# Performance work log

Measured on AMD Instinct MI355X. Metric: run time of the kernel, lower is better.

The kernel has to match this reference:

```python
import jax, jax.numpy as jnp
import numpy as np

N = 8192      # nodes
E = 262144    # edges (avg degree 32)
NFEAT = 1024
NHID = 512
ZDIM = 32


def _uniform(key, shape, stdv):
    return jax.random.uniform(key, shape, jnp.float32, -stdv, stdv)


def setup_inputs() -> dict:
    key = jax.random.key(0)
    ks = jax.random.split(key, 10)
    x = jax.random.normal(ks[0], (N, NFEAT), jnp.float32)
    adj_rows = jnp.sort(jax.random.randint(ks[1], (E,), 0, N))
    adj_cols = jax.random.randint(ks[2], (E,), 0, N)
    # positive edge weights, roughly row-normalized (avg degree 32)
    adj_vals = jax.random.uniform(ks[3], (E,), jnp.float32) / 32.0
    s0 = 1.0 / np.sqrt(NHID).astype(np.float32)
    s1 = 1.0 / np.sqrt(ZDIM).astype(np.float32)
    W0 = _uniform(ks[4], (NFEAT, NHID), s0)
    b0 = _uniform(ks[5], (NHID,), s0)
    W1 = _uniform(ks[6], (NHID, ZDIM), s1)
    b1 = _uniform(ks[7], (ZDIM,), s1)
    W2 = _uniform(ks[8], (NHID, ZDIM), s1)
    b2 = _uniform(ks[9], (ZDIM,), s1)
    return dict(x=x, adj_vals=adj_vals, W0=W0, b0=b0, W1=W1, b1=b1,
                W2=W2, b2=b2, adj_rows=adj_rows, adj_cols=adj_cols)


def _spmm(rows, cols, vals, mat):
    # sparse [N,N] @ dense [N,D] via gather + segment_sum
    return jax.ops.segment_sum(vals[:, None] * mat[cols], rows, num_segments=N)


def reference(x, adj_vals, W0, b0, W1, b1, W2, b2, adj_rows, adj_cols):
    # GraphConvolution: spmm(adj, x @ W) + b  (eval mode: dropout is identity)
    h = jax.nn.relu(_spmm(adj_rows, adj_cols, adj_vals, x @ W0) + b0)
    mu = jax.nn.relu(_spmm(adj_rows, adj_cols, adj_vals, h @ W1) + b1)
    logvar = jax.nn.relu(_spmm(adj_rows, adj_cols, adj_vals, h @ W2) + b2)
    z = mu  # reparameterize in eval mode returns mu
    adj_recon = jax.nn.sigmoid(z @ z.T)  # [N, N] inner-product decoder
    return adj_recon, z, mu, logvar
```

## Files before the change

### kernel.cpp

```cpp
#include <hip/hip_runtime.h>
#include <hip/hip_bf16.h>

typedef __bf16 bf16_t;
typedef __bf16 bf16x8 __attribute__((ext_vector_type(8)));
typedef float f32x4 __attribute__((ext_vector_type(4)));

#define NN 8192
#define EE 262144
#define NF 1024
#define NH 512
#define ZD 32

__global__ __launch_bounds__(256) void k_cvt(const float* __restrict__ in,
                                             bf16_t* __restrict__ out, int n8) {
  int i = blockIdx.x * 256 + threadIdx.x;
  if (i >= n8) return;
  const float4 a = ((const float4*)in)[i * 2];
  const float4 b = ((const float4*)in)[i * 2 + 1];
  bf16x8 o;
  o[0] = (bf16_t)a.x; o[1] = (bf16_t)a.y; o[2] = (bf16_t)a.z; o[3] = (bf16_t)a.w;
  o[4] = (bf16_t)b.x; o[5] = (bf16_t)b.y; o[6] = (bf16_t)b.z; o[7] = (bf16_t)b.w;
  ((bf16x8*)out)[i] = o;
}

__global__ __launch_bounds__(256) void k_transpose_cvt(const float* __restrict__ in,
                                                       bf16_t* __restrict__ out,
                                                       int R, int C) {
  __shared__ float tile[32][33];
  const int c0 = blockIdx.x * 32, r0 = blockIdx.y * 32;
  const int tx = threadIdx.x & 31, ty = threadIdx.x >> 5;
  #pragma unroll
  for (int i = ty; i < 32; i += 8)
    tile[i][tx] = in[(size_t)(r0 + i) * C + (c0 + tx)];
  __syncthreads();
  #pragma unroll
  for (int i = ty; i < 32; i += 8)
    out[(size_t)(c0 + i) * R + (r0 + tx)] = (bf16_t)tile[tx][i];
}

__global__ void k_rowptr(const int* __restrict__ rows, int* __restrict__ rp,
                         int n, int e) {
  int r = blockIdx.x * 256 + threadIdx.x;
  if (r > n) return;
  if (r == n) { rp[n] = e; return; }
  int lo = 0, hi = e;
  while (lo < hi) { int mid = (lo + hi) >> 1; if (rows[mid] < r) lo = mid + 1; else hi = mid; }
  rp[r] = lo;
}

__global__ __launch_bounds__(256) void k_gemm_bt_128x128(
    const bf16_t* __restrict__ A, const bf16_t* __restrict__ Bt,
    float* __restrict__ C, int M, int N, int K) {
  __shared__ bf16_t As[128 * 32];
  __shared__ bf16_t Bs[128 * 32];
  const int tid = threadIdx.x;
  const int lane = tid & 63, wave = tid >> 6;
  const int wx = wave & 1, wy = wave >> 1;
  const int m0 = blockIdx.y * 128, n0 = blockIdx.x * 128;
  const int q = lane >> 4, ml = lane & 15;

  const int sr = tid >> 2, ss = tid & 3;
  const int sw_lo = sr * 32 + ((ss ^ (sr & 3)) * 8);
  const int sw_hi = sw_lo + 64 * 32;

  int a_off[4], b_off[4];
  #pragma unroll
  for (int i = 0; i < 4; ++i) {
    int m = wy * 64 + i * 16 + ml;
    a_off[i] = m * 32 + ((q ^ (m & 3)) * 8);
    int n = wx * 64 + i * 16 + ml;
    b_off[i] = n * 32 + ((q ^ (n & 3)) * 8);
  }

  f32x4 acc[4][4];
  #pragma unroll
  for (int i = 0; i < 4; ++i)
    #pragma unroll
    for (int j = 0; j < 4; ++j)
      acc[i][j] = (f32x4){0.f, 0.f, 0.f, 0.f};

  const bf16_t* ga = A + (size_t)(m0 + sr) * K + ss * 8;
  const bf16_t* gb = Bt + (size_t)(n0 + sr) * K + ss * 8;
  const size_t stride64 = (size_t)64 * K;

  for (int k0 = 0; k0 < K; k0 += 32) {
    int4 va0 = *(const int4*)(ga + k0);
    int4 va1 = *(const int4*)(ga + stride64 + k0);
    int4 vb0 = *(const int4*)(gb + k0);
    int4 vb1 = *(const int4*)(gb + stride64 + k0);
    __syncthreads();
    *(int4*)(&As[sw_lo]) = va0;
    *(int4*)(&As[sw_hi]) = va1;
    *(int4*)(&Bs[sw_lo]) = vb0;
    *(int4*)(&Bs[sw_hi]) = vb1;
    __syncthreads();
    bf16x8 af[4], bfr[4];
    #pragma unroll
    for (int i = 0; i < 4; ++i) af[i] = *(const bf16x8*)(&As[a_off[i]]);
    #pragma unroll
    for (int j = 0; j < 4; ++j) bfr[j] = *(const bf16x8*)(&Bs[b_off[j]]);
    #pragma unroll
    for (int i = 0; i < 4; ++i)
      #pragma unroll
      for (int j = 0; j < 4; ++j)
        acc[i][j] = __builtin_amdgcn_mfma_f32_16x16x32_bf16(af[i], bfr[j], acc[i][j], 0, 0, 0);
  }

  #pragma unroll
  for (int i = 0; i < 4; ++i) {
    const int row = m0 + wy * 64 + i * 16 + q * 4;
    #pragma unroll
    for (int j = 0; j < 4; ++j) {
      const int col = n0 + wx * 64 + j * 16 + ml;
      #pragma unroll
      for (int r = 0; r < 4; ++r)
        C[(size_t)(row + r) * N + col] = acc[i][j][r];
    }
  }
}

__global__ __launch_bounds__(256) void k_gemm_bt_128x64(
    const bf16_t* __restrict__ A, const bf16_t* __restrict__ Bt,
    float* __restrict__ C, int M, int N, int K) {
  __shared__ bf16_t As[128 * 32];
  __shared__ bf16_t Bs[64 * 32];
  const int tid = threadIdx.x;
  const int lane = tid & 63, wave = tid >> 6;
  const int m0 = blockIdx.y * 128;
  const int q = lane >> 4, ml = lane & 15;
  const int sr = tid >> 2, ss = tid & 3;
  const int sw_lo = sr * 32 + ((ss ^ (sr & 3)) * 8);
  const int sw_hi = sw_lo + 64 * 32;

  int a_off[2], b_off[4];
  #pragma unroll
  for (int i = 0; i < 2; ++i) {
    int m = wave * 32 + i * 16 + ml;
    a_off[i] = m * 32 + ((q ^ (m & 3)) * 8);
  }
  #pragma unroll
  for (int j = 0; j < 4; ++j) {
    int n = j * 16 + ml;
    b_off[j] = n * 32 + ((q ^ (n & 3)) * 8);
  }

  f32x4 acc[2][4];
  #pragma unroll
  for (int i = 0; i < 2; ++i)
    #pragma unroll
    for (int j = 0; j < 4; ++j)
      acc[i][j] = (f32x4){0.f, 0.f, 0.f, 0.f};

  const bf16_t* ga = A + (size_t)(m0 + sr) * K + ss * 8;
  const bf16_t* gb = Bt + (size_t)sr * K + ss * 8;
  const size_t stride64 = (size_t)64 * K;

  for (int k0 = 0; k0 < K; k0 += 32) {
    int4 va0 = *(const int4*)(ga + k0);
    int4 va1 = *(const int4*)(ga + stride64 + k0);
    int4 vb0 = *(const int4*)(gb + k0);
    __syncthreads();
    *(int4*)(&As[sw_lo]) = va0;
    *(int4*)(&As[sw_hi]) = va1;
    *(int4*)(&Bs[sw_lo]) = vb0;
    __syncthreads();
    bf16x8 af[2], bfr[4];
    #pragma unroll
    for (int i = 0; i < 2; ++i) af[i] = *(const bf16x8*)(&As[a_off[i]]);
    #pragma unroll
    for (int j = 0; j < 4; ++j) bfr[j] = *(const bf16x8*)(&Bs[b_off[j]]);
    #pragma unroll
    for (int i = 0; i < 2; ++i)
      #pragma unroll
      for (int j = 0; j < 4; ++j)
        acc[i][j] = __builtin_amdgcn_mfma_f32_16x16x32_bf16(af[i], bfr[j], acc[i][j], 0, 0, 0);
  }

  #pragma unroll
  for (int i = 0; i < 2; ++i) {
    const int row = m0 + wave * 32 + i * 16 + q * 4;
    #pragma unroll
    for (int j = 0; j < 4; ++j) {
      const int col = j * 16 + ml;
      #pragma unroll
      for (int r = 0; r < 4; ++r)
        C[(size_t)(row + r) * N + col] = acc[i][j][r];
    }
  }
}

__global__ __launch_bounds__(256) void k_spmm_h(
    const int* __restrict__ rp, const int* __restrict__ cols,
    const float* __restrict__ vals, const float* __restrict__ XW0,
    const float* __restrict__ b0, bf16_t* __restrict__ h) {
  const int r = blockIdx.x;
  const int t = threadIdx.x;
  const int beg = rp[r], end = rp[r + 1];
  float acc0 = 0.f, acc1 = 0.f;
  for (int e = beg; e < end; ++e) {
    const float v = vals[e];
    const float* src = XW0 + (size_t)cols[e] * NH;
    acc0 += v * src[t];
    acc1 += v * src[t + 256];
  }
  acc0 += b0[t];
  acc1 += b0[t + 256];
  h[(size_t)r * NH + t]       = (bf16_t)fmaxf(acc0, 0.f);
  h[(size_t)r * NH + t + 256] = (bf16_t)fmaxf(acc1, 0.f);
}

__global__ __launch_bounds__(64) void k_spmm_z(
    const int* __restrict__ rp, const int* __restrict__ cols,
    const float* __restrict__ vals, const float* __restrict__ HW,
    const float* __restrict__ b1, const float* __restrict__ b2,
    float* __restrict__ out_z, float* __restrict__ out_mu,
    float* __restrict__ out_lv, bf16_t* __restrict__ zb) {
  const int r = blockIdx.x;
  const int t = threadIdx.x;
  const int beg = rp[r], end = rp[r + 1];
  float acc = 0.f;
  for (int e = beg; e < end; ++e)
    acc += vals[e] * HW[(size_t)cols[e] * 64 + t];
  const float b = (t < ZD) ? b1[t] : b2[t - ZD];
  const float v = fmaxf(acc + b, 0.f);
  if (t < ZD) {
    out_mu[(size_t)r * ZD + t] = v;
    out_z[(size_t)r * ZD + t] = v;
    zb[(size_t)r * ZD + t] = (bf16_t)v;
  } else {
    out_lv[(size_t)r * ZD + (t - ZD)] = v;
  }
}

__global__ __launch_bounds__(256) void k_decoder(const bf16_t* __restrict__ Z,
                                                 float* __restrict__ out) {
  __shared__ bf16_t Zr[128 * 32];
  __shared__ bf16_t Zc[128 * 32];
  const int tid = threadIdx.x;
  const int lane = tid & 63, wave = tid >> 6;
  const int wx = wave & 1, wy = wave >> 1;
  const int m0 = blockIdx.y * 128, n0 = blockIdx.x * 128;
  const int q = lane >> 4, ml = lane & 15;
  const int sr = tid >> 2, ss = tid & 3;
  const int sw_lo = sr * 32 + ((ss ^ (sr & 3)) * 8);
  const int sw_hi = sw_lo + 64 * 32;

  *(int4*)(&Zr[sw_lo]) = *((const int4*)(Z + (size_t)(m0 + sr) * ZD) + ss);
  *(int4*)(&Zr[sw_hi]) = *((const int4*)(Z + (size_t)(m0 + sr + 64) * ZD) + ss);
  *(int4*)(&Zc[sw_lo]) = *((const int4*)(Z + (size_t)(n0 + sr) * ZD) + ss);
  *(int4*)(&Zc[sw_hi]) = *((const int4*)(Z + (size_t)(n0 + sr + 64) * ZD) + ss);
  __syncthreads();

  bf16x8 af[4], bfr[4];
  #pragma unroll
  for (int i = 0; i < 4; ++i) {
    int m = wy * 64 + i * 16 + ml;
    af[i] = *(const bf16x8*)(&Zr[m * 32 + ((q ^ (m & 3)) * 8)]);
    int n = wx * 64 + i * 16 + ml;
    bfr[i] = *(const bf16x8*)(&Zc[n * 32 + ((q ^ (n & 3)) * 8)]);
  }
  const f32x4 zero = (f32x4){0.f, 0.f, 0.f, 0.f};
  #pragma unroll
  for (int i = 0; i < 4; ++i) {
    const int row = m0 + wy * 64 + i * 16 + q * 4;
    #pragma unroll
    for (int j = 0; j < 4; ++j) {
      const int col = n0 + wx * 64 + j * 16 + ml;
      f32x4 c = __builtin_amdgcn_mfma_f32_16x16x32_bf16(af[i], bfr[j], zero, 0, 0, 0);
      #pragma unroll
      for (int r = 0; r < 4; ++r)
        out[(size_t)(row + r) * NN + col] = 1.f / (1.f + __expf(-c[r]));
    }
  }
}

extern "C" void kernel_launch(void* const* d_in, const int* in_sizes, int n_in,
                              void* d_out, int out_size, void* d_ws, size_t ws_size,
                              hipStream_t stream) {
  const float* x        = (const float*)d_in[0];
  const float* adj_vals = (const float*)d_in[1];
  const float* W0       = (const float*)d_in[2];
  const float* b0       = (const float*)d_in[3];
  const float* W1       = (const float*)d_in[4];
  const float* b1       = (const float*)d_in[5];
  const float* W2       = (const float*)d_in[6];
  const float* b2       = (const float*)d_in[7];
  const int* adj_rows   = (const int*)d_in[8];
  const int* adj_cols   = (const int*)d_in[9];

  char* ws = (char*)d_ws;
  float*  XW0 = (float*)(ws);
  float*  HW  = (float*)(ws + 16777216);
  bf16_t* h   = (bf16_t*)(ws + 18874368);
  bf16_t* W0t = (bf16_t*)(ws + 27262976);
  bf16_t* Wct = (bf16_t*)(ws + 28311552);
  bf16_t* xb  = (bf16_t*)(ws + 28377088);
  bf16_t* zb  = (bf16_t*)(ws + 45154304);
  int*    rp  = (int*)(ws + 45678592);

  float* out     = (float*)d_out;
  float* out_adj = out;
  float* out_z   = out + (size_t)NN * NN;
  float* out_mu  = out_z + (size_t)NN * ZD;
  float* out_lv  = out_mu + (size_t)NN * ZD;

  k_cvt<<<(NN * NF / 8 + 255) / 256, 256, 0, stream>>>(x, xb, NN * NF / 8);
  k_transpose_cvt<<<dim3(NH / 32, NF / 32), 256, 0, stream>>>(W0, W0t, NF, NH);
  k_transpose_cvt<<<dim3(ZD / 32, NH / 32), 256, 0, stream>>>(W1, Wct, NH, ZD);
  k_transpose_cvt<<<dim3(ZD / 32, NH / 32), 256, 0, stream>>>(W2, Wct + ZD * NH, NH, ZD);
  k_rowptr<<<33, 256, 0, stream>>>(adj_rows, rp, NN, EE);

  k_gemm_bt_128x128<<<dim3(NH / 128, NN / 128), 256, 0, stream>>>(xb, W0t, XW0, NN, NH, NF);
  k_spmm_h<<<NN, 256, 0, stream>>>(rp, adj_cols, adj_vals, XW0, b0, h);

  k_gemm_bt_128x64<<<dim3(1, NN / 128), 256, 0, stream>>>(h, Wct, HW, NN, 64, NH);
  k_spmm_z<<<NN, 64, 0, stream>>>(rp, adj_cols, adj_vals, HW, b1, b2, out_z, out_mu, out_lv, zb);

  k_decoder<<<dim3(NN / 128, NN / 128), 256, 0, stream>>>(zb, out_adj);
}
```

Baseline: 466.3 us.

## Store XW0 in bf16 and gather packed pairs in SpMM over column chunks

The first GEMM now writes its output in bf16 instead of fp32, which halves the intermediate that the first SpMM gathers. k_spmm_h is restructured into four 64-thread blocks per row, each reading packed bf16 pairs as 32-bit words, with the edge loop unrolled by two. The second SpMM is unrolled the same way, and the two small W1/W2 transposes are merged into one launch. The cost is extra bf16 rounding of XW0 before aggregation, plus four times as many blocks, each of which re-reads the row pointers and edge data.

Result: faster. 435.5 us (-6.6%).

```diff
diff --git a/kernel.cpp b/kernel.cpp
--- a/kernel.cpp
+++ b/kernel.cpp
@@ -38,6 +38,23 @@
     out[(size_t)(c0 + i) * R + (r0 + tx)] = (bf16_t)tile[tx][i];
 }
 
+__global__ __launch_bounds__(256) void k_transpose_w12(const float* __restrict__ W1,
+                                                       const float* __restrict__ W2,
+                                                       bf16_t* __restrict__ out) {
+  __shared__ float tile[32][33];
+  const float* in = blockIdx.z ? W2 : W1;
+  bf16_t* o = out + (size_t)blockIdx.z * ZD * NH;
+  const int r0 = blockIdx.y * 32;
+  const int tx = threadIdx.x & 31, ty = threadIdx.x >> 5;
+  #pragma unroll
+  for (int i = ty; i < 32; i += 8)
+    tile[i][tx] = in[(size_t)(r0 + i) * ZD + tx];
+  __syncthreads();
+  #pragma unroll
+  for (int i = ty; i < 32; i += 8)
+    o[(size_t)(i)*NH + (r0 + tx)] = (bf16_t)tile[tx][i];
+}
+
 __global__ void k_rowptr(const int* __restrict__ rows, int* __restrict__ rp,
                          int n, int e) {
   int r = blockIdx.x * 256 + threadIdx.x;
@@ -50,7 +67,7 @@
 
 __global__ __launch_bounds__(256) void k_gemm_bt_128x128(
     const bf16_t* __restrict__ A, const bf16_t* __restrict__ Bt,
-    float* __restrict__ C, int M, int N, int K) {
+    bf16_t* __restrict__ C, int M, int N, int K) {
   __shared__ bf16_t As[128 * 32];
   __shared__ bf16_t Bs[128 * 32];
   const int tid = threadIdx.x;
@@ -114,7 +131,7 @@
       const int col = n0 + wx * 64 + j * 16 + ml;
       #pragma unroll
       for (int r = 0; r < 4; ++r)
-        C[(size_t)(row + r) * N + col] = acc[i][j][r];
+        C[(size_t)(row + r) * N + col] = (bf16_t)acc[i][j][r];
     }
   }
 }
@@ -189,24 +206,38 @@
   }
 }
 
-__global__ __launch_bounds__(256) void k_spmm_h(
+__global__ __launch_bounds__(64) void k_spmm_h(
     const int* __restrict__ rp, const int* __restrict__ cols,
-    const float* __restrict__ vals, const float* __restrict__ XW0,
+    const float* __restrict__ vals, const unsigned int* __restrict__ XW0b,
     const float* __restrict__ b0, bf16_t* __restrict__ h) {
-  const int r = blockIdx.x;
+  const int row = blockIdx.x >> 2, chunk = blockIdx.x & 3;
   const int t = threadIdx.x;
-  const int beg = rp[r], end = rp[r + 1];
-  float acc0 = 0.f, acc1 = 0.f;
-  for (int e = beg; e < end; ++e) {
-    const float v = vals[e];
-    const float* src = XW0 + (size_t)cols[e] * NH;
-    acc0 += v * src[t];
-    acc1 += v * src[t + 256];
-  }
-  acc0 += b0[t];
-  acc1 += b0[t + 256];
-  h[(size_t)r * NH + t]       = (bf16_t)fmaxf(acc0, 0.f);
-  h[(size_t)r * NH + t + 256] = (bf16_t)fmaxf(acc1, 0.f);
+  const unsigned int* tab = XW0b + chunk * 64 + t;
+  int e = rp[row];
+  const int end = rp[row + 1];
+  float a0 = 0.f, a1 = 0.f;
+  for (; e + 1 < end; e += 2) {
+    const int c0 = cols[e], c1 = cols[e + 1];
+    const float v0 = vals[e], v1 = vals[e + 1];
+    const unsigned int p0 = tab[(size_t)c0 * 256];
+    const unsigned int p1 = tab[(size_t)c1 * 256];
+    a0 += v0 * __uint_as_float(p0 << 16);
+    a1 += v0 * __uint_as_float(p0 & 0xffff0000u);
+    a0 += v1 * __uint_as_float(p1 << 16);
+    a1 += v1 * __uint_as_float(p1 & 0xffff0000u);
+  }
+  if (e < end) {
+    const float v0 = vals[e];
+    const unsigned int p0 = tab[(size_t)cols[e] * 256];
+    a0 += v0 * __uint_as_float(p0 << 16);
+    a1 += v0 * __uint_as_float(p0 & 0xffff0000u);
+  }
+  const int d = chunk * 128 + t * 2;
+  a0 += b0[d];
+  a1 += b0[d + 1];
+  bf16_t* o = h + (size_t)row * NH + d;
+  o[0] = (bf16_t)fmaxf(a0, 0.f);
+  o[1] = (bf16_t)fmaxf(a1, 0.f);
 }
 
 __global__ __launch_bounds__(64) void k_spmm_z(
@@ -217,10 +248,16 @@
     float* __restrict__ out_lv, bf16_t* __restrict__ zb) {
   const int r = blockIdx.x;
   const int t = threadIdx.x;
-  const int beg = rp[r], end = rp[r + 1];
+  int e = rp[r];
+  const int end = rp[r + 1];
   float acc = 0.f;
-  for (int e = beg; e < end; ++e)
-    acc += vals[e] * HW[(size_t)cols[e] * 64 + t];
+  for (; e + 1 < end; e += 2) {
+    const float v0 = vals[e], v1 = vals[e + 1];
+    const float s0 = HW[(size_t)cols[e] * 64 + t];
+    const float s1 = HW[(size_t)cols[e + 1] * 64 + t];
+    acc += v0 * s0 + v1 * s1;
+  }
+  if (e < end) acc += vals[e] * HW[(size_t)cols[e] * 64 + t];
   const float b = (t < ZD) ? b1[t] : b2[t - ZD];
   const float v = fmaxf(acc + b, 0.f);
   if (t < ZD) {
@@ -289,14 +326,14 @@
   const int* adj_cols   = (const int*)d_in[9];
 
   char* ws = (char*)d_ws;
-  float*  XW0 = (float*)(ws);
-  float*  HW  = (float*)(ws + 16777216);
-  bf16_t* h   = (bf16_t*)(ws + 18874368);
-  bf16_t* W0t = (bf16_t*)(ws + 27262976);
-  bf16_t* Wct = (bf16_t*)(ws + 28311552);
-  bf16_t* xb  = (bf16_t*)(ws + 28377088);
-  bf16_t* zb  = (bf16_t*)(ws + 45154304);
-  int*    rp  = (int*)(ws + 45678592);
+  bf16_t* XW0b = (bf16_t*)(ws);
+  float*  HW   = (float*)(ws + 8388608);
+  bf16_t* h    = (bf16_t*)(ws + 10485760);
+  bf16_t* W0t  = (bf16_t*)(ws + 18874368);
+  bf16_t* Wct  = (bf16_t*)(ws + 19922944);
+  bf16_t* xb   = (bf16_t*)(ws + 19988480);
+  bf16_t* zb   = (bf16_t*)(ws + 36765696);
+  int*    rp   = (int*)(ws + 37289984);
 
   float* out     = (float*)d_out;
   float* out_adj = out;
@@ -306,12 +343,12 @@
 
   k_cvt<<<(NN * NF / 8 + 255) / 256, 256, 0, stream>>>(x, xb, NN * NF / 8);
   k_transpose_cvt<<<dim3(NH / 32, NF / 32), 256, 0, stream>>>(W0, W0t, NF, NH);
-  k_transpose_cvt<<<dim3(ZD / 32, NH / 32), 256, 0, stream>>>(W1, Wct, NH, ZD);
-  k_transpose_cvt<<<dim3(ZD / 32, NH / 32), 256, 0, stream>>>(W2, Wct + ZD * NH, NH, ZD);
+  k_transpose_w12<<<dim3(1, NH / 32, 2), 256, 0, stream>>>(W1, W2, Wct);
   k_rowptr<<<33, 256, 0, stream>>>(adj_rows, rp, NN, EE);
 
-  k_gemm_bt_128x128<<<dim3(NH / 128, NN / 128), 256, 0, stream>>>(xb, W0t, XW0, NN, NH, NF);
-  k_spmm_h<<<NN, 256, 0, stream>>>(rp, adj_cols, adj_vals, XW0, b0, h);
+  k_gemm_bt_128x128<<<dim3(NH / 128, NN / 128), 256, 0, stream>>>(xb, W0t, XW0b, NN, NH, NF);
+  k_spmm_h<<<NN * 4, 64, 0, stream>>>(rp, adj_cols, adj_vals,
+                                      (const unsigned int*)XW0b, b0, h);
 
   k_gemm_bt_128x64<<<dim3(1, NN / 128), 256, 0, stream>>>(h, Wct, HW, NN, 64, NH);
   k_spmm_z<<<NN, 64, 0, stream>>>(rp, adj_cols, adj_vals, HW, b1, b2, out_z, out_mu, out_lv, zb);
```
